# Performance work log

Hardware: AMD Instinct MI355X
Metric: run time of the kernel (lower is better)

Reference implementation:

```python
import jax, jax.numpy as jnp
import numpy as np

N_NODES = 100000
N_EDGES = 1600000
IN_FEATS = 128
OUT_FEATS = 128


def setup_inputs() -> dict:
    key = jax.random.key(0)
    ks = jax.random.split(key, 8)
    feat = jax.random.normal(ks[0], (N_NODES, IN_FEATS), dtype=jnp.float32)
    weight = jax.random.normal(ks[1], (IN_FEATS, OUT_FEATS), dtype=jnp.float32) * (1.0 / np.sqrt(IN_FEATS))
    bias = jnp.zeros((OUT_FEATS,), dtype=jnp.float32)
    s = 1.0 / np.sqrt(OUT_FEATS)
    w_ih = jax.random.uniform(ks[2], (3 * OUT_FEATS, IN_FEATS), dtype=jnp.float32, minval=-s, maxval=s)
    w_hh = jax.random.uniform(ks[3], (3 * OUT_FEATS, OUT_FEATS), dtype=jnp.float32, minval=-s, maxval=s)
    b_ih = jax.random.uniform(ks[4], (3 * OUT_FEATS,), dtype=jnp.float32, minval=-s, maxval=s)
    b_hh = jax.random.uniform(ks[5], (3 * OUT_FEATS,), dtype=jnp.float32, minval=-s, maxval=s)
    src = jax.random.randint(ks[6], (N_EDGES,), 0, N_NODES, dtype=jnp.int32)
    dst = jax.random.randint(ks[7], (N_EDGES,), 0, N_NODES, dtype=jnp.int32)
    return {"feat": feat, "weight": weight, "bias": bias,
            "w_ih": w_ih, "w_hh": w_hh, "b_ih": b_ih, "b_hh": b_hh,
            "src": src, "dst": dst}


def reference(feat, weight, bias, w_ih, w_hh, b_ih, b_hh, src, dst):
    n = feat.shape[0]
    # symmetric-ish GCN norm: in-degree^{-1/2}, clamped at 1
    deg = jax.ops.segment_sum(jnp.ones(dst.shape, feat.dtype), dst, num_segments=n)
    norm = jnp.power(jnp.clip(deg, 1.0, None), -0.5)[:, None]  # [N,1]
    featn = feat * norm
    # copy_src + sum aggregation (SpMM via gather + segment_sum), then matmul
    agg = jax.ops.segment_sum(featn[src], dst, num_segments=n)  # [N, in]
    rst = agg @ weight                                           # [N, out]
    rst = rst * norm + bias
    # GRUCell(input=featn, hidden=rst)
    gi = featn @ w_ih.T + b_ih   # [N, 3*out]
    gh = rst @ w_hh.T + b_hh     # [N, 3*out]
    i_r, i_z, i_n = jnp.split(gi, 3, axis=1)
    h_r, h_z, h_n = jnp.split(gh, 3, axis=1)
    r = jax.nn.sigmoid(i_r + h_r)
    z = jax.nn.sigmoid(i_z + h_z)
    nn_ = jnp.tanh(i_n + r * h_n)
    return (1.0 - z) * nn_ + z * rst
```

## Files before the change

kernel.cpp:

```cpp
#include <hip/hip_runtime.h>
#include <hip/hip_bf16.h>
#include <math.h>

#define N_NODES 100000
#define N_EDGES 1600000
#define F 128


#define WS_FEATN_OFF 8001536
#define WS_WTI_OFF   59201536
#define WS_WTH_OFF   59398144
#define WS_NEED_FULL (WS_WTH_OFF + 196608)

__global__ __launch_bounds__(256) void k_degree(const int* __restrict__ dst,
                                                int* __restrict__ deg) {
    int i = blockIdx.x * 256 + threadIdx.x;
    if (i < N_EDGES) atomicAdd(&deg[dst[i]], 1);
}

#define SCAN_B 512
#define SCAN_NB 196

__global__ __launch_bounds__(SCAN_B) void k_scan1(const int* __restrict__ deg,
                                                  int* __restrict__ bsum) {
    __shared__ int s[SCAN_B];
    int t = threadIdx.x;
    int i = blockIdx.x * SCAN_B + t;
    s[t] = (i < N_NODES) ? deg[i] : 0;
    __syncthreads();
    for (int o = SCAN_B / 2; o > 0; o >>= 1) {
        if (t < o) s[t] += s[t + o];
        __syncthreads();
    }
    if (t == 0) bsum[blockIdx.x] = s[0];
}

__global__ __launch_bounds__(256) void k_scan2(int* __restrict__ bsum) {
    __shared__ int s[256];
    int t = threadIdx.x;
    int v = (t < SCAN_NB) ? bsum[t] : 0;
    s[t] = v;
    __syncthreads();
    for (int o = 1; o < 256; o <<= 1) {
        int x = (t >= o) ? s[t - o] : 0;
        __syncthreads();
        s[t] += x;
        __syncthreads();
    }
    if (t < SCAN_NB) bsum[t] = (t == 0) ? 0 : s[t - 1];
}

__global__ __launch_bounds__(SCAN_B) void k_scan3(const int* __restrict__ deg,
                                                  const int* __restrict__ bsum,
                                                  int* __restrict__ offs,
                                                  float* __restrict__ norm,
                                                  int* __restrict__ cursor) {
    __shared__ int s[SCAN_B];
    int t = threadIdx.x;
    int i = blockIdx.x * SCAN_B + t;
    int v = (i < N_NODES) ? deg[i] : 0;
    s[t] = v;
    __syncthreads();
    for (int o = 1; o < SCAN_B; o <<= 1) {
        int x = (t >= o) ? s[t - o] : 0;
        __syncthreads();
        s[t] += x;
        __syncthreads();
    }
    if (i < N_NODES) {
        offs[i] = bsum[blockIdx.x] + s[t] - v;
        norm[i] = rsqrtf(fmaxf((float)v, 1.0f));
        cursor[i] = 0;
    }
    if (blockIdx.x == 0 && t == 0) offs[N_NODES] = N_EDGES;
}

__global__ __launch_bounds__(256) void k_fill(const int* __restrict__ src,
                                              const int* __restrict__ dst,
                                              const int* __restrict__ offs,
                                              int* __restrict__ cursor,
                                              int* __restrict__ ssrc) {
    int i = blockIdx.x * 256 + threadIdx.x;
    if (i < N_EDGES) {
        int d = dst[i];
        int p = atomicAdd(&cursor[d], 1);
        ssrc[offs[d] + p] = src[i];
    }
}

__global__ __launch_bounds__(256) void k_featn(const float* __restrict__ feat,
                                               const float* __restrict__ norm,
                                               float* __restrict__ featn) {
    int idx = blockIdx.x * 256 + threadIdx.x;
    int row = idx >> 5;
    float nv = norm[row];
    float4 v = ((const float4*)feat)[idx];
    v.x *= nv; v.y *= nv; v.z *= nv; v.w *= nv;
    ((float4*)featn)[idx] = v;
}

__global__ __launch_bounds__(256) void k_wt(const float* __restrict__ w_ih,
                                            const float* __restrict__ w_hh,
                                            float* __restrict__ wT_ih,
                                            float* __restrict__ wT_hh) {
    __shared__ float tile[32][33];
    int b = blockIdx.x;
    const float* w = (b < 48) ? w_ih : w_hh;
    float* wT      = (b < 48) ? wT_ih : wT_hh;
    int bb = (b < 48) ? b : b - 48;
    int rt = bb >> 2, ct = bb & 3;
    int r0 = rt * 32, c0 = ct * 32;
    int tr = threadIdx.x >> 5, tc = threadIdx.x & 31;
#pragma unroll
    for (int i = 0; i < 32; i += 8)
        tile[tr + i][tc] = w[(r0 + tr + i) * 128 + c0 + tc];
    __syncthreads();
#pragma unroll
    for (int i = 0; i < 32; i += 8)
        wT[(c0 + tr + i) * 384 + r0 + tc] = tile[tc][tr + i];
}

#define ROWS 8
template <bool PRE>
__global__ __launch_bounds__(256, 4) void k_fused(
    const float* __restrict__ fsrc, const float* __restrict__ norm,
    const int* __restrict__ offs, const int* __restrict__ ssrc,
    const float* __restrict__ W, const float* __restrict__ bias,
    const float* __restrict__ wih_, const float* __restrict__ whh_,
    const float* __restrict__ b_ih, const float* __restrict__ b_hh,
    float* __restrict__ out) {
    __shared__ float sagg[ROWS][F];
    __shared__ float sfeat[ROWS][F];
    __shared__ float srst[ROWS][F];
    __shared__ float snorm[ROWS];

    int t = threadIdx.x;
    int row0 = blockIdx.x * ROWS;

    if (t < ROWS) snorm[t] = norm[row0 + t];
    {
        int r = t >> 5, c = t & 31;
        float4 f = ((const float4*)(fsrc + (size_t)(row0 + r) * F))[c];
        if (!PRE) {
            float nv = norm[row0 + r];
            f.x *= nv; f.y *= nv; f.z *= nv; f.w *= nv;
        }
        ((float4*)&sfeat[r][0])[c] = f;
    }

    int wave = t >> 6, lane = t & 63;
    int hf = lane >> 5, sub = lane & 31;
    for (int ln = wave; ln < ROWS; ln += 4) {
        int node = row0 + ln;
        int beg = offs[node], end = offs[node + 1];
        float4 acc = make_float4(0.f, 0.f, 0.f, 0.f);
        int e = beg;
        for (; e + 7 < end; e += 8) {
            int s0 = ssrc[e + 0 + hf];
            int s1 = ssrc[e + 2 + hf];
            int s2 = ssrc[e + 4 + hf];
            int s3 = ssrc[e + 6 + hf];
            float4 v0 = *(const float4*)(fsrc + (size_t)s0 * F + sub * 4);
            float4 v1 = *(const float4*)(fsrc + (size_t)s1 * F + sub * 4);
            float4 v2 = *(const float4*)(fsrc + (size_t)s2 * F + sub * 4);
            float4 v3 = *(const float4*)(fsrc + (size_t)s3 * F + sub * 4);
            if (PRE) {
                acc.x += (v0.x + v1.x) + (v2.x + v3.x);
                acc.y += (v0.y + v1.y) + (v2.y + v3.y);
                acc.z += (v0.z + v1.z) + (v2.z + v3.z);
                acc.w += (v0.w + v1.w) + (v2.w + v3.w);
            } else {
                float n0 = norm[s0], n1 = norm[s1], n2 = norm[s2], n3 = norm[s3];
                acc.x = fmaf(v0.x, n0, acc.x); acc.y = fmaf(v0.y, n0, acc.y);
                acc.z = fmaf(v0.z, n0, acc.z); acc.w = fmaf(v0.w, n0, acc.w);
                acc.x = fmaf(v1.x, n1, acc.x); acc.y = fmaf(v1.y, n1, acc.y);
                acc.z = fmaf(v1.z, n1, acc.z); acc.w = fmaf(v1.w, n1, acc.w);
                acc.x = fmaf(v2.x, n2, acc.x); acc.y = fmaf(v2.y, n2, acc.y);
                acc.z = fmaf(v2.z, n2, acc.z); acc.w = fmaf(v2.w, n2, acc.w);
                acc.x = fmaf(v3.x, n3, acc.x); acc.y = fmaf(v3.y, n3, acc.y);
                acc.z = fmaf(v3.z, n3, acc.z); acc.w = fmaf(v3.w, n3, acc.w);
            }
        }
        for (; e < end; e += 2) {
            int edge = e + hf;
            if (edge < end) {
                int s0 = ssrc[edge];
                float4 v0 = *(const float4*)(fsrc + (size_t)s0 * F + sub * 4);
                float n0 = PRE ? 1.0f : norm[s0];
                acc.x = fmaf(v0.x, n0, acc.x); acc.y = fmaf(v0.y, n0, acc.y);
                acc.z = fmaf(v0.z, n0, acc.z); acc.w = fmaf(v0.w, n0, acc.w);
            }
        }
        acc.x += __shfl_xor(acc.x, 32, 64);
        acc.y += __shfl_xor(acc.y, 32, 64);
        acc.z += __shfl_xor(acc.z, 32, 64);
        acc.w += __shfl_xor(acc.w, 32, 64);
        if (hf == 0) *(float4*)&sagg[ln][sub * 4] = acc;
    }
    __syncthreads();

    int j = t & 127;
    int rg = (t >> 7) * 4;
    {
        float acc[4] = {0, 0, 0, 0};
        for (int k = 0; k < F; k += 4) {
            float w0 = W[(k + 0) * F + j];
            float w1 = W[(k + 1) * F + j];
            float w2 = W[(k + 2) * F + j];
            float w3 = W[(k + 3) * F + j];
#pragma unroll
            for (int r = 0; r < 4; ++r) {
                float4 a = *(const float4*)&sagg[rg + r][k];
                acc[r] = fmaf(a.x, w0, acc[r]);
                acc[r] = fmaf(a.y, w1, acc[r]);
                acc[r] = fmaf(a.z, w2, acc[r]);
                acc[r] = fmaf(a.w, w3, acc[r]);
            }
        }
        float bj = bias[j];
#pragma unroll
        for (int r = 0; r < 4; ++r) {
            srst[rg + r][j] = acc[r] * snorm[rg + r] + bj;
        }
    }
    __syncthreads();

    float accr[4] = {0, 0, 0, 0};
    float accz[4] = {0, 0, 0, 0};
    float accin[4] = {0, 0, 0, 0};
    float acchn[4] = {0, 0, 0, 0};

    if (PRE) {
        for (int k = 0; k < F; k += 4) {
            float wir[4], wiz[4], win[4], whr[4], whz[4], whn[4];
#pragma unroll
            for (int kk = 0; kk < 4; ++kk) {
                const float* wik = wih_ + (size_t)(k + kk) * 384 + j;
                const float* whk = whh_ + (size_t)(k + kk) * 384 + j;
                wir[kk] = wik[0]; wiz[kk] = wik[128]; win[kk] = wik[256];
                whr[kk] = whk[0]; whz[kk] = whk[128]; whn[kk] = whk[256];
            }
#pragma unroll
            for (int r = 0; r < 4; ++r) {
                float4 a = *(const float4*)&sfeat[rg + r][k];
                float4 h = *(const float4*)&srst[rg + r][k];
                accr[r] = fmaf(a.x, wir[0], accr[r]); accr[r] = fmaf(h.x, whr[0], accr[r]);
                accr[r] = fmaf(a.y, wir[1], accr[r]); accr[r] = fmaf(h.y, whr[1], accr[r]);
                accr[r] = fmaf(a.z, wir[2], accr[r]); accr[r] = fmaf(h.z, whr[2], accr[r]);
                accr[r] = fmaf(a.w, wir[3], accr[r]); accr[r] = fmaf(h.w, whr[3], accr[r]);
                accz[r] = fmaf(a.x, wiz[0], accz[r]); accz[r] = fmaf(h.x, whz[0], accz[r]);
                accz[r] = fmaf(a.y, wiz[1], accz[r]); accz[r] = fmaf(h.y, whz[1], accz[r]);
                accz[r] = fmaf(a.z, wiz[2], accz[r]); accz[r] = fmaf(h.z, whz[2], accz[r]);
                accz[r] = fmaf(a.w, wiz[3], accz[r]); accz[r] = fmaf(h.w, whz[3], accz[r]);
                accin[r] = fmaf(a.x, win[0], accin[r]); accin[r] = fmaf(a.y, win[1], accin[r]);
                accin[r] = fmaf(a.z, win[2], accin[r]); accin[r] = fmaf(a.w, win[3], accin[r]);
                acchn[r] = fmaf(h.x, whn[0], acchn[r]); acchn[r] = fmaf(h.y, whn[1], acchn[r]);
                acchn[r] = fmaf(h.z, whn[2], acchn[r]); acchn[r] = fmaf(h.w, whn[3], acchn[r]);
            }
        }
    } else {
        const float* wirp = wih_ + (size_t)(j + 0) * F;
        const float* wizp = wih_ + (size_t)(j + 128) * F;
        const float* winp = wih_ + (size_t)(j + 256) * F;
        const float* whrp = whh_ + (size_t)(j + 0) * F;
        const float* whzp = whh_ + (size_t)(j + 128) * F;
        const float* whnp = whh_ + (size_t)(j + 256) * F;
        for (int k = 0; k < F; k += 4) {
            float4 bir = *(const float4*)(wirp + k);
            float4 biz = *(const float4*)(wizp + k);
            float4 bin = *(const float4*)(winp + k);
            float4 bhr = *(const float4*)(whrp + k);
            float4 bhz = *(const float4*)(whzp + k);
            float4 bhn = *(const float4*)(whnp + k);
#pragma unroll
            for (int r = 0; r < 4; ++r) {
                float4 a = *(const float4*)&sfeat[rg + r][k];
                float4 h = *(const float4*)&srst[rg + r][k];
                accr[r] = fmaf(a.x, bir.x, accr[r]); accr[r] = fmaf(h.x, bhr.x, accr[r]);
                accr[r] = fmaf(a.y, bir.y, accr[r]); accr[r] = fmaf(h.y, bhr.y, accr[r]);
                accr[r] = fmaf(a.z, bir.z, accr[r]); accr[r] = fmaf(h.z, bhr.z, accr[r]);
                accr[r] = fmaf(a.w, bir.w, accr[r]); accr[r] = fmaf(h.w, bhr.w, accr[r]);
                accz[r] = fmaf(a.x, biz.x, accz[r]); accz[r] = fmaf(h.x, bhz.x, accz[r]);
                accz[r] = fmaf(a.y, biz.y, accz[r]); accz[r] = fmaf(h.y, bhz.y, accz[r]);
                accz[r] = fmaf(a.z, biz.z, accz[r]); accz[r] = fmaf(h.z, bhz.z, accz[r]);
                accz[r] = fmaf(a.w, biz.w, accz[r]); accz[r] = fmaf(h.w, bhz.w, accz[r]);
                accin[r] = fmaf(a.x, bin.x, accin[r]); accin[r] = fmaf(a.y, bin.y, accin[r]);
                accin[r] = fmaf(a.z, bin.z, accin[r]); accin[r] = fmaf(a.w, bin.w, accin[r]);
                acchn[r] = fmaf(h.x, bhn.x, acchn[r]); acchn[r] = fmaf(h.y, bhn.y, acchn[r]);
                acchn[r] = fmaf(h.z, bhn.z, acchn[r]); acchn[r] = fmaf(h.w, bhn.w, acchn[r]);
            }
        }
    }

    float Brz = b_ih[j] + b_hh[j];
    float Bzz = b_ih[j + 128] + b_hh[j + 128];
    float Bin = b_ih[j + 256], Bhn = b_hh[j + 256];
#pragma unroll
    for (int r = 0; r < 4; ++r) {
        int row = row0 + rg + r;
        float rr = 1.0f / (1.0f + __expf(-(accr[r] + Brz)));
        float zz = 1.0f / (1.0f + __expf(-(accz[r] + Bzz)));
        float nn = tanhf(accin[r] + Bin + rr * (acchn[r] + Bhn));
        float rstv = srst[rg + r][j];
        out[(size_t)row * F + j] = (1.0f - zz) * nn + zz * rstv;
    }
}

extern "C" void kernel_launch(void* const* d_in, const int* in_sizes, int n_in,
                              void* d_out, int out_size, void* d_ws, size_t ws_size,
                              hipStream_t stream) {
    const float* feat   = (const float*)d_in[0];
    const float* weight = (const float*)d_in[1];
    const float* bias   = (const float*)d_in[2];
    const float* w_ih   = (const float*)d_in[3];
    const float* w_hh   = (const float*)d_in[4];
    const float* b_ih   = (const float*)d_in[5];
    const float* b_hh   = (const float*)d_in[6];
    const int*   src    = (const int*)d_in[7];
    const int*   dst    = (const int*)d_in[8];
    float* out = (float*)d_out;

    char* ws = (char*)d_ws;
    int*   deg    = (int*)(ws + 0);
    float* norm   = (float*)(ws + 400000);
    int*   offs   = (int*)(ws + 800000);
    int*   cursor = (int*)(ws + 1200016);
    int*   ssrc   = (int*)(ws + 1600016);
    int*   bsum   = (int*)(ws + 8000016);
    float* featn  = (float*)(ws + WS_FEATN_OFF);
    float* wT_ih  = (float*)(ws + WS_WTI_OFF);
    float* wT_hh  = (float*)(ws + WS_WTH_OFF);

    hipMemsetAsync(deg, 0, N_NODES * sizeof(int), stream);

    k_degree<<<(N_EDGES + 255) / 256, 256, 0, stream>>>(dst, deg);
    k_scan1<<<SCAN_NB, SCAN_B, 0, stream>>>(deg, bsum);
    k_scan2<<<1, 256, 0, stream>>>(bsum);
    k_scan3<<<SCAN_NB, SCAN_B, 0, stream>>>(deg, bsum, offs, norm, cursor);
    k_fill<<<(N_EDGES + 255) / 256, 256, 0, stream>>>(src, dst, offs, cursor, ssrc);

    if (ws_size >= WS_NEED_FULL) {
        k_wt<<<96, 256, 0, stream>>>(w_ih, w_hh, wT_ih, wT_hh);
        k_featn<<<(N_NODES * F / 4) / 256, 256, 0, stream>>>(feat, norm, featn);
        k_fused<true><<<N_NODES / ROWS, 256, 0, stream>>>(featn, norm, offs, ssrc,
                                                          weight, bias, wT_ih, wT_hh,
                                                          b_ih, b_hh, out);
    } else {
        k_fused<false><<<N_NODES / ROWS, 256, 0, stream>>>(feat, norm, offs, ssrc,
                                                           weight, bias, w_ih, w_hh,
                                                           b_ih, b_hh, out);
    }
}
```

Measured before the change: 830.6 us.

## Pack GRU weights into interleaved float4/float2 layout and double rows per block

```diff
diff --git a/kernel.cpp b/kernel.cpp
--- a/kernel.cpp
+++ b/kernel.cpp
@@ -8,9 +8,9 @@
 
 
 #define WS_FEATN_OFF 8001536
-#define WS_WTI_OFF   59201536
-#define WS_WTH_OFF   59398144
-#define WS_NEED_FULL (WS_WTH_OFF + 196608)
+#define WS_WPA_OFF   59201536
+#define WS_WPB_OFF   59463680
+#define WS_NEED_FULL (WS_WPB_OFF + 131072)
 
 __global__ __launch_bounds__(256) void k_degree(const int* __restrict__ dst,
                                                 int* __restrict__ deg) {
@@ -99,33 +99,31 @@
     ((float4*)featn)[idx] = v;
 }
 
-__global__ __launch_bounds__(256) void k_wt(const float* __restrict__ w_ih,
-                                            const float* __restrict__ w_hh,
-                                            float* __restrict__ wT_ih,
-                                            float* __restrict__ wT_hh) {
-    __shared__ float tile[32][33];
-    int b = blockIdx.x;
-    const float* w = (b < 48) ? w_ih : w_hh;
-    float* wT      = (b < 48) ? wT_ih : wT_hh;
-    int bb = (b < 48) ? b : b - 48;
-    int rt = bb >> 2, ct = bb & 3;
-    int r0 = rt * 32, c0 = ct * 32;
-    int tr = threadIdx.x >> 5, tc = threadIdx.x & 31;
-#pragma unroll
-    for (int i = 0; i < 32; i += 8)
-        tile[tr + i][tc] = w[(r0 + tr + i) * 128 + c0 + tc];
-    __syncthreads();
-#pragma unroll
-    for (int i = 0; i < 32; i += 8)
-        wT[(c0 + tr + i) * 384 + r0 + tc] = tile[tc][tr + i];
-}
-
-#define ROWS 8
+__global__ __launch_bounds__(256) void k_pack(const float* __restrict__ w_ih,
+                                              const float* __restrict__ w_hh,
+                                              float4* __restrict__ wPa,
+                                              float2* __restrict__ wPb) {
+    int idx = blockIdx.x * 256 + threadIdx.x;
+    int k = idx >> 7, j = idx & 127;
+    float4 a;
+    a.x = w_ih[j * 128 + k];
+    a.y = w_ih[(j + 128) * 128 + k];
+    a.z = w_ih[(j + 256) * 128 + k];
+    a.w = w_hh[j * 128 + k];
+    float2 b;
+    b.x = w_hh[(j + 128) * 128 + k];
+    b.y = w_hh[(j + 256) * 128 + k];
+    wPa[idx] = a;
+    wPb[idx] = b;
+}
+
+#define ROWS 16
 template <bool PRE>
-__global__ __launch_bounds__(256, 4) void k_fused(
+__global__ __launch_bounds__(512, 4) void k_fused(
     const float* __restrict__ fsrc, const float* __restrict__ norm,
     const int* __restrict__ offs, const int* __restrict__ ssrc,
     const float* __restrict__ W, const float* __restrict__ bias,
+    const float4* __restrict__ wPa_, const float2* __restrict__ wPb_,
     const float* __restrict__ wih_, const float* __restrict__ whh_,
     const float* __restrict__ b_ih, const float* __restrict__ b_hh,
     float* __restrict__ out) {
@@ -150,7 +148,7 @@
 
     int wave = t >> 6, lane = t & 63;
     int hf = lane >> 5, sub = lane & 31;
-    for (int ln = wave; ln < ROWS; ln += 4) {
+    for (int ln = wave; ln < ROWS; ln += 8) {
         int node = row0 + ln;
         int beg = offs[node], end = offs[node + 1];
         float4 acc = make_float4(0.f, 0.f, 0.f, 0.f);
@@ -231,31 +229,33 @@
     float acchn[4] = {0, 0, 0, 0};
 
     if (PRE) {
+        const float4* pa = wPa_ + j;
+        const float2* pb = wPb_ + j;
         for (int k = 0; k < F; k += 4) {
-            float wir[4], wiz[4], win[4], whr[4], whz[4], whn[4];
-#pragma unroll
-            for (int kk = 0; kk < 4; ++kk) {
-                const float* wik = wih_ + (size_t)(k + kk) * 384 + j;
-                const float* whk = whh_ + (size_t)(k + kk) * 384 + j;
-                wir[kk] = wik[0]; wiz[kk] = wik[128]; win[kk] = wik[256];
-                whr[kk] = whk[0]; whz[kk] = whk[128]; whn[kk] = whk[256];
-            }
+            float4 A0 = pa[(k + 0) * 128];
+            float4 A1 = pa[(k + 1) * 128];
+            float4 A2 = pa[(k + 2) * 128];
+            float4 A3 = pa[(k + 3) * 128];
+            float2 B0 = pb[(k + 0) * 128];
+            float2 B1 = pb[(k + 1) * 128];
+            float2 B2 = pb[(k + 2) * 128];
+            float2 B3 = pb[(k + 3) * 128];
 #pragma unroll
             for (int r = 0; r < 4; ++r) {
                 float4 a = *(const float4*)&sfeat[rg + r][k];
                 float4 h = *(const float4*)&srst[rg + r][k];
-                accr[r] = fmaf(a.x, wir[0], accr[r]); accr[r] = fmaf(h.x, whr[0], accr[r]);
-                accr[r] = fmaf(a.y, wir[1], accr[r]); accr[r] = fmaf(h.y, whr[1], accr[r]);
-                accr[r] = fmaf(a.z, wir[2], accr[r]); accr[r] = fmaf(h.z, whr[2], accr[r]);
-                accr[r] = fmaf(a.w, wir[3], accr[r]); accr[r] = fmaf(h.w, whr[3], accr[r]);
-                accz[r] = fmaf(a.x, wiz[0], accz[r]); accz[r] = fmaf(h.x, whz[0], accz[r]);
-                accz[r] = fmaf(a.y, wiz[1], accz[r]); accz[r] = fmaf(h.y, whz[1], accz[r]);
-                accz[r] = fmaf(a.z, wiz[2], accz[r]); accz[r] = fmaf(h.z, whz[2], accz[r]);
-                accz[r] = fmaf(a.w, wiz[3], accz[r]); accz[r] = fmaf(h.w, whz[3], accz[r]);
-                accin[r] = fmaf(a.x, win[0], accin[r]); accin[r] = fmaf(a.y, win[1], accin[r]);
-                accin[r] = fmaf(a.z, win[2], accin[r]); accin[r] = fmaf(a.w, win[3], accin[r]);
-                acchn[r] = fmaf(h.x, whn[0], acchn[r]); acchn[r] = fmaf(h.y, whn[1], acchn[r]);
-                acchn[r] = fmaf(h.z, whn[2], acchn[r]); acchn[r] = fmaf(h.w, whn[3], acchn[r]);
+                accr[r] = fmaf(a.x, A0.x, accr[r]); accr[r] = fmaf(h.x, A0.w, accr[r]);
+                accr[r] = fmaf(a.y, A1.x, accr[r]); accr[r] = fmaf(h.y, A1.w, accr[r]);
+                accr[r] = fmaf(a.z, A2.x, accr[r]); accr[r] = fmaf(h.z, A2.w, accr[r]);
+                accr[r] = fmaf(a.w, A3.x, accr[r]); accr[r] = fmaf(h.w, A3.w, accr[r]);
+                accz[r] = fmaf(a.x, A0.y, accz[r]); accz[r] = fmaf(h.x, B0.x, accz[r]);
+                accz[r] = fmaf(a.y, A1.y, accz[r]); accz[r] = fmaf(h.y, B1.x, accz[r]);
+                accz[r] = fmaf(a.z, A2.y, accz[r]); accz[r] = fmaf(h.z, B2.x, accz[r]);
+                accz[r] = fmaf(a.w, A3.y, accz[r]); accz[r] = fmaf(h.w, B3.x, accz[r]);
+                accin[r] = fmaf(a.x, A0.z, accin[r]); accin[r] = fmaf(a.y, A1.z, accin[r]);
+                accin[r] = fmaf(a.z, A2.z, accin[r]); accin[r] = fmaf(a.w, A3.z, accin[r]);
+                acchn[r] = fmaf(h.x, B0.y, acchn[r]); acchn[r] = fmaf(h.y, B1.y, acchn[r]);
+                acchn[r] = fmaf(h.z, B2.y, acchn[r]); acchn[r] = fmaf(h.w, B3.y, acchn[r]);
             }
         }
     } else {
@@ -321,15 +321,15 @@
     float* out = (float*)d_out;
 
     char* ws = (char*)d_ws;
-    int*   deg    = (int*)(ws + 0);
-    float* norm   = (float*)(ws + 400000);
-    int*   offs   = (int*)(ws + 800000);
-    int*   cursor = (int*)(ws + 1200016);
-    int*   ssrc   = (int*)(ws + 1600016);
-    int*   bsum   = (int*)(ws + 8000016);
-    float* featn  = (float*)(ws + WS_FEATN_OFF);
-    float* wT_ih  = (float*)(ws + WS_WTI_OFF);
-    float* wT_hh  = (float*)(ws + WS_WTH_OFF);
+    int*    deg    = (int*)(ws + 0);
+    float*  norm   = (float*)(ws + 400000);
+    int*    offs   = (int*)(ws + 800000);
+    int*    cursor = (int*)(ws + 1200016);
+    int*    ssrc   = (int*)(ws + 1600016);
+    int*    bsum   = (int*)(ws + 8000016);
+    float*  featn  = (float*)(ws + WS_FEATN_OFF);
+    float4* wPa    = (float4*)(ws + WS_WPA_OFF);
+    float2* wPb    = (float2*)(ws + WS_WPB_OFF);
 
     hipMemsetAsync(deg, 0, N_NODES * sizeof(int), stream);
 
@@ -340,14 +340,16 @@
     k_fill<<<(N_EDGES + 255) / 256, 256, 0, stream>>>(src, dst, offs, cursor, ssrc);
 
     if (ws_size >= WS_NEED_FULL) {
-        k_wt<<<96, 256, 0, stream>>>(w_ih, w_hh, wT_ih, wT_hh);
+        k_pack<<<64, 256, 0, stream>>>(w_ih, w_hh, wPa, wPb);
         k_featn<<<(N_NODES * F / 4) / 256, 256, 0, stream>>>(feat, norm, featn);
-        k_fused<true><<<N_NODES / ROWS, 256, 0, stream>>>(featn, norm, offs, ssrc,
-                                                          weight, bias, wT_ih, wT_hh,
+        k_fused<true><<<N_NODES / ROWS, 512, 0, stream>>>(featn, norm, offs, ssrc,
+                                                          weight, bias, wPa, wPb,
+                                                          nullptr, nullptr,
                                                           b_ih, b_hh, out);
     } else {
-        k_fused<false><<<N_NODES / ROWS, 256, 0, stream>>>(feat, norm, offs, ssrc,
-                                                           weight, bias, w_ih, w_hh,
+        k_fused<false><<<N_NODES / ROWS, 512, 0, stream>>>(feat, norm, offs, ssrc,
+                                                           weight, bias, nullptr, nullptr,
+                                                           w_ih, w_hh,
                                                            b_ih, b_hh, out);
     }
 }
```

Result: no change. 823.1 us (-0.9%).

## Use split-bf16 MFMA for GCN and GRU matmuls with 32-row tiles

Applied to the files above, without the earlier changes.

```diff
diff --git a/kernel.cpp b/kernel.cpp
--- a/kernel.cpp
+++ b/kernel.cpp
@@ -8,9 +8,32 @@
 
 
 #define WS_FEATN_OFF 8001536
-#define WS_WTI_OFF   59201536
-#define WS_WTH_OFF   59398144
-#define WS_NEED_FULL (WS_WTH_OFF + 196608)
+#define WS_WIHH 1200016
+#define WS_WIHL 1298320
+#define WS_WTH  59201536
+#define WS_WTL  59234304
+#define WS_WHHH 59267072
+#define WS_WHHL 59365376
+
+using s8v = __attribute__((ext_vector_type(8))) short;
+using f4v = __attribute__((ext_vector_type(4))) float;
+
+__device__ __forceinline__ void bsplit(float x, unsigned short& h, unsigned short& l) {
+    unsigned bx = __float_as_uint(x);
+    unsigned rh = bx + 0x7FFFu + ((bx >> 16) & 1u);
+    h = (unsigned short)(rh >> 16);
+    float fh = __uint_as_float(((unsigned)h) << 16);
+    float lo = x - fh;
+    unsigned bl = __float_as_uint(lo);
+    unsigned rl = bl + 0x7FFFu + ((bl >> 16) & 1u);
+    l = (unsigned short)(rl >> 16);
+}
+
+__device__ __forceinline__ unsigned long long pack4(unsigned short a, unsigned short b,
+                                                    unsigned short c, unsigned short d) {
+    return (unsigned long long)a | ((unsigned long long)b << 16) |
+           ((unsigned long long)c << 32) | ((unsigned long long)d << 48);
+}
 
 __global__ __launch_bounds__(256) void k_degree(const int* __restrict__ dst,
                                                 int* __restrict__ deg) {
@@ -99,58 +122,68 @@
     ((float4*)featn)[idx] = v;
 }
 
-__global__ __launch_bounds__(256) void k_wt(const float* __restrict__ w_ih,
-                                            const float* __restrict__ w_hh,
-                                            float* __restrict__ wT_ih,
-                                            float* __restrict__ wT_hh) {
-    __shared__ float tile[32][33];
-    int b = blockIdx.x;
-    const float* w = (b < 48) ? w_ih : w_hh;
-    float* wT      = (b < 48) ? wT_ih : wT_hh;
-    int bb = (b < 48) ? b : b - 48;
-    int rt = bb >> 2, ct = bb & 3;
-    int r0 = rt * 32, c0 = ct * 32;
-    int tr = threadIdx.x >> 5, tc = threadIdx.x & 31;
-#pragma unroll
-    for (int i = 0; i < 32; i += 8)
-        tile[tr + i][tc] = w[(r0 + tr + i) * 128 + c0 + tc];
-    __syncthreads();
-#pragma unroll
-    for (int i = 0; i < 32; i += 8)
-        wT[(c0 + tr + i) * 384 + r0 + tc] = tile[tc][tr + i];
-}
-
-#define ROWS 8
-template <bool PRE>
-__global__ __launch_bounds__(256, 4) void k_fused(
-    const float* __restrict__ fsrc, const float* __restrict__ norm,
+__global__ __launch_bounds__(256) void k_packw(const float* __restrict__ weight,
+                                               const float* __restrict__ w_ih,
+                                               const float* __restrict__ w_hh,
+                                               unsigned short* __restrict__ WtH,
+                                               unsigned short* __restrict__ WtL,
+                                               unsigned short* __restrict__ wihH,
+                                               unsigned short* __restrict__ wihL,
+                                               unsigned short* __restrict__ whhH,
+                                               unsigned short* __restrict__ whhL) {
+    int idx = blockIdx.x * 256 + threadIdx.x;
+    unsigned short h, l;
+    if (idx < 16384) {
+        int n = idx >> 7, k = idx & 127;
+        bsplit(weight[k * 128 + n], h, l);
+        WtH[idx] = h; WtL[idx] = l;
+    } else if (idx < 65536) {
+        int i2 = idx - 16384;
+        bsplit(w_ih[i2], h, l);
+        wihH[i2] = h; wihL[i2] = l;
+    } else {
+        int i2 = idx - 65536;
+        bsplit(w_hh[i2], h, l);
+        whhH[i2] = h; whhL[i2] = l;
+    }
+}
+
+#define ROWS 32
+__global__ __launch_bounds__(512, 2) void k_fused(
+    const float* __restrict__ featn, const float* __restrict__ norm,
     const int* __restrict__ offs, const int* __restrict__ ssrc,
-    const float* __restrict__ W, const float* __restrict__ bias,
-    const float* __restrict__ wih_, const float* __restrict__ whh_,
-    const float* __restrict__ b_ih, const float* __restrict__ b_hh,
-    float* __restrict__ out) {
-    __shared__ float sagg[ROWS][F];
-    __shared__ float sfeat[ROWS][F];
-    __shared__ float srst[ROWS][F];
+    const unsigned short* __restrict__ WtH, const unsigned short* __restrict__ WtL,
+    const unsigned short* __restrict__ wihH, const unsigned short* __restrict__ wihL,
+    const unsigned short* __restrict__ whhH, const unsigned short* __restrict__ whhL,
+    const float* __restrict__ bias, const float* __restrict__ b_ih,
+    const float* __restrict__ b_hh, float* __restrict__ out) {
+    __shared__ __align__(16) unsigned short sfH[4096], sfL[4096];
+    __shared__ __align__(16) unsigned short sgH[4096], sgL[4096];
+    __shared__ __align__(16) unsigned short srH[4096], srL[4096];
     __shared__ float snorm[ROWS];
 
     int t = threadIdx.x;
+    int l = t & 63, w = t >> 6, g = l >> 4;
     int row0 = blockIdx.x * ROWS;
 
     if (t < ROWS) snorm[t] = norm[row0 + t];
-    {
-        int r = t >> 5, c = t & 31;
-        float4 f = ((const float4*)(fsrc + (size_t)(row0 + r) * F))[c];
-        if (!PRE) {
-            float nv = norm[row0 + r];
-            f.x *= nv; f.y *= nv; f.z *= nv; f.w *= nv;
-        }
-        ((float4*)&sfeat[r][0])[c] = f;
-    }
-
-    int wave = t >> 6, lane = t & 63;
-    int hf = lane >> 5, sub = lane & 31;
-    for (int ln = wave; ln < ROWS; ln += 4) {
+
+#pragma unroll
+    for (int u = 0; u < 2; ++u) {
+        int idx = u * 512 + t;
+        int r = idx >> 5, c = idx & 31;
+        float4 f = ((const float4*)(featn + (size_t)(row0 + r) * F))[c];
+        int k0 = c * 4;
+        int pos = (r >> 4) * 2048 + (k0 >> 3) * 128 + (r & 15) * 8 + (k0 & 7);
+        unsigned short h0, l0, h1, l1, h2, l2, h3, l3;
+        bsplit(f.x, h0, l0); bsplit(f.y, h1, l1);
+        bsplit(f.z, h2, l2); bsplit(f.w, h3, l3);
+        *(unsigned long long*)(&sfH[pos]) = pack4(h0, h1, h2, h3);
+        *(unsigned long long*)(&sfL[pos]) = pack4(l0, l1, l2, l3);
+    }
+
+    int hf = l >> 5, sub = l & 31;
+    for (int ln = w; ln < ROWS; ln += 8) {
         int node = row0 + ln;
         int beg = offs[node], end = offs[node + 1];
         float4 acc = make_float4(0.f, 0.f, 0.f, 0.f);
@@ -160,149 +193,125 @@
             int s1 = ssrc[e + 2 + hf];
             int s2 = ssrc[e + 4 + hf];
             int s3 = ssrc[e + 6 + hf];
-            float4 v0 = *(const float4*)(fsrc + (size_t)s0 * F + sub * 4);
-            float4 v1 = *(const float4*)(fsrc + (size_t)s1 * F + sub * 4);
-            float4 v2 = *(const float4*)(fsrc + (size_t)s2 * F + sub * 4);
-            float4 v3 = *(const float4*)(fsrc + (size_t)s3 * F + sub * 4);
-            if (PRE) {
-                acc.x += (v0.x + v1.x) + (v2.x + v3.x);
-                acc.y += (v0.y + v1.y) + (v2.y + v3.y);
-                acc.z += (v0.z + v1.z) + (v2.z + v3.z);
-                acc.w += (v0.w + v1.w) + (v2.w + v3.w);
-            } else {
-                float n0 = norm[s0], n1 = norm[s1], n2 = norm[s2], n3 = norm[s3];
-                acc.x = fmaf(v0.x, n0, acc.x); acc.y = fmaf(v0.y, n0, acc.y);
-                acc.z = fmaf(v0.z, n0, acc.z); acc.w = fmaf(v0.w, n0, acc.w);
-                acc.x = fmaf(v1.x, n1, acc.x); acc.y = fmaf(v1.y, n1, acc.y);
-                acc.z = fmaf(v1.z, n1, acc.z); acc.w = fmaf(v1.w, n1, acc.w);
-                acc.x = fmaf(v2.x, n2, acc.x); acc.y = fmaf(v2.y, n2, acc.y);
-                acc.z = fmaf(v2.z, n2, acc.z); acc.w = fmaf(v2.w, n2, acc.w);
-                acc.x = fmaf(v3.x, n3, acc.x); acc.y = fmaf(v3.y, n3, acc.y);
-                acc.z = fmaf(v3.z, n3, acc.z); acc.w = fmaf(v3.w, n3, acc.w);
-            }
+            float4 v0 = *(const float4*)(featn + (size_t)s0 * F + sub * 4);
+            float4 v1 = *(const float4*)(featn + (size_t)s1 * F + sub * 4);
+            float4 v2 = *(const float4*)(featn + (size_t)s2 * F + sub * 4);
+            float4 v3 = *(const float4*)(featn + (size_t)s3 * F + sub * 4);
+            acc.x += (v0.x + v1.x) + (v2.x + v3.x);
+            acc.y += (v0.y + v1.y) + (v2.y + v3.y);
+            acc.z += (v0.z + v1.z) + (v2.z + v3.z);
+            acc.w += (v0.w + v1.w) + (v2.w + v3.w);
         }
         for (; e < end; e += 2) {
             int edge = e + hf;
             if (edge < end) {
                 int s0 = ssrc[edge];
-                float4 v0 = *(const float4*)(fsrc + (size_t)s0 * F + sub * 4);
-                float n0 = PRE ? 1.0f : norm[s0];
-                acc.x = fmaf(v0.x, n0, acc.x); acc.y = fmaf(v0.y, n0, acc.y);
-                acc.z = fmaf(v0.z, n0, acc.z); acc.w = fmaf(v0.w, n0, acc.w);
+                float4 v0 = *(const float4*)(featn + (size_t)s0 * F + sub * 4);
+                acc.x += v0.x; acc.y += v0.y; acc.z += v0.z; acc.w += v0.w;
             }
         }
         acc.x += __shfl_xor(acc.x, 32, 64);
         acc.y += __shfl_xor(acc.y, 32, 64);
         acc.z += __shfl_xor(acc.z, 32, 64);
         acc.w += __shfl_xor(acc.w, 32, 64);
-        if (hf == 0) *(float4*)&sagg[ln][sub * 4] = acc;
-    }
-    __syncthreads();
-
-    int j = t & 127;
-    int rg = (t >> 7) * 4;
-    {
-        float acc[4] = {0, 0, 0, 0};
-        for (int k = 0; k < F; k += 4) {
-            float w0 = W[(k + 0) * F + j];
-            float w1 = W[(k + 1) * F + j];
-            float w2 = W[(k + 2) * F + j];
-            float w3 = W[(k + 3) * F + j];
-#pragma unroll
-            for (int r = 0; r < 4; ++r) {
-                float4 a = *(const float4*)&sagg[rg + r][k];
-                acc[r] = fmaf(a.x, w0, acc[r]);
-                acc[r] = fmaf(a.y, w1, acc[r]);
-                acc[r] = fmaf(a.z, w2, acc[r]);
-                acc[r] = fmaf(a.w, w3, acc[r]);
-            }
-        }
-        float bj = bias[j];
-#pragma unroll
-        for (int r = 0; r < 4; ++r) {
-            srst[rg + r][j] = acc[r] * snorm[rg + r] + bj;
-        }
-    }
-    __syncthreads();
-
-    float accr[4] = {0, 0, 0, 0};
-    float accz[4] = {0, 0, 0, 0};
-    float accin[4] = {0, 0, 0, 0};
-    float acchn[4] = {0, 0, 0, 0};
-
-    if (PRE) {
-        for (int k = 0; k < F; k += 4) {
-            float wir[4], wiz[4], win[4], whr[4], whz[4], whn[4];
-#pragma unroll
-            for (int kk = 0; kk < 4; ++kk) {
-                const float* wik = wih_ + (size_t)(k + kk) * 384 + j;
-                const float* whk = whh_ + (size_t)(k + kk) * 384 + j;
-                wir[kk] = wik[0]; wiz[kk] = wik[128]; win[kk] = wik[256];
-                whr[kk] = whk[0]; whz[kk] = whk[128]; whn[kk] = whk[256];
-            }
-#pragma unroll
-            for (int r = 0; r < 4; ++r) {
-                float4 a = *(const float4*)&sfeat[rg + r][k];
-                float4 h = *(const float4*)&srst[rg + r][k];
-                accr[r] = fmaf(a.x, wir[0], accr[r]); accr[r] = fmaf(h.x, whr[0], accr[r]);
-                accr[r] = fmaf(a.y, wir[1], accr[r]); accr[r] = fmaf(h.y, whr[1], accr[r]);
-                accr[r] = fmaf(a.z, wir[2], accr[r]); accr[r] = fmaf(h.z, whr[2], accr[r]);
-                accr[r] = fmaf(a.w, wir[3], accr[r]); accr[r] = fmaf(h.w, whr[3], accr[r]);
-                accz[r] = fmaf(a.x, wiz[0], accz[r]); accz[r] = fmaf(h.x, whz[0], accz[r]);
-                accz[r] = fmaf(a.y, wiz[1], accz[r]); accz[r] = fmaf(h.y, whz[1], accz[r]);
-                accz[r] = fmaf(a.z, wiz[2], accz[r]); accz[r] = fmaf(h.z, whz[2], accz[r]);
-                accz[r] = fmaf(a.w, wiz[3], accz[r]); accz[r] = fmaf(h.w, whz[3], accz[r]);
-                accin[r] = fmaf(a.x, win[0], accin[r]); accin[r] = fmaf(a.y, win[1], accin[r]);
-                accin[r] = fmaf(a.z, win[2], accin[r]); accin[r] = fmaf(a.w, win[3], accin[r]);
-                acchn[r] = fmaf(h.x, whn[0], acchn[r]); acchn[r] = fmaf(h.y, whn[1], acchn[r]);
-                acchn[r] = fmaf(h.z, whn[2], acchn[r]); acchn[r] = fmaf(h.w, whn[3], acchn[r]);
-            }
-        }
-    } else {
-        const float* wirp = wih_ + (size_t)(j + 0) * F;
-        const float* wizp = wih_ + (size_t)(j + 128) * F;
-        const float* winp = wih_ + (size_t)(j + 256) * F;
-        const float* whrp = whh_ + (size_t)(j + 0) * F;
-        const float* whzp = whh_ + (size_t)(j + 128) * F;
-        const float* whnp = whh_ + (size_t)(j + 256) * F;
-        for (int k = 0; k < F; k += 4) {
-            float4 bir = *(const float4*)(wirp + k);
-            float4 biz = *(const float4*)(wizp + k);
-            float4 bin = *(const float4*)(winp + k);
-            float4 bhr = *(const float4*)(whrp + k);
-            float4 bhz = *(const float4*)(whzp + k);
-            float4 bhn = *(const float4*)(whnp + k);
-#pragma unroll
-            for (int r = 0; r < 4; ++r) {
-                float4 a = *(const float4*)&sfeat[rg + r][k];
-                float4 h = *(const float4*)&srst[rg + r][k];
-                accr[r] = fmaf(a.x, bir.x, accr[r]); accr[r] = fmaf(h.x, bhr.x, accr[r]);
-                accr[r] = fmaf(a.y, bir.y, accr[r]); accr[r] = fmaf(h.y, bhr.y, accr[r]);
-                accr[r] = fmaf(a.z, bir.z, accr[r]); accr[r] = fmaf(h.z, bhr.z, accr[r]);
-                accr[r] = fmaf(a.w, bir.w, accr[r]); accr[r] = fmaf(h.w, bhr.w, accr[r]);
-                accz[r] = fmaf(a.x, biz.x, accz[r]); accz[r] = fmaf(h.x, bhz.x, accz[r]);
-                accz[r] = fmaf(a.y, biz.y, accz[r]); accz[r] = fmaf(h.y, bhz.y, accz[r]);
-                accz[r] = fmaf(a.z, biz.z, accz[r]); accz[r] = fmaf(h.z, bhz.z, accz[r]);
-                accz[r] = fmaf(a.w, biz.w, accz[r]); accz[r] = fmaf(h.w, bhz.w, accz[r]);
-                accin[r] = fmaf(a.x, bin.x, accin[r]); accin[r] = fmaf(a.y, bin.y, accin[r]);
-                accin[r] = fmaf(a.z, bin.z, accin[r]); accin[r] = fmaf(a.w, bin.w, accin[r]);
-                acchn[r] = fmaf(h.x, bhn.x, acchn[r]); acchn[r] = fmaf(h.y, bhn.y, acchn[r]);
-                acchn[r] = fmaf(h.z, bhn.z, acchn[r]); acchn[r] = fmaf(h.w, bhn.w, acchn[r]);
-            }
-        }
-    }
-
-    float Brz = b_ih[j] + b_hh[j];
-    float Bzz = b_ih[j + 128] + b_hh[j + 128];
-    float Bin = b_ih[j + 256], Bhn = b_hh[j + 256];
-#pragma unroll
-    for (int r = 0; r < 4; ++r) {
-        int row = row0 + rg + r;
-        float rr = 1.0f / (1.0f + __expf(-(accr[r] + Brz)));
-        float zz = 1.0f / (1.0f + __expf(-(accz[r] + Bzz)));
-        float nn = tanhf(accin[r] + Bin + rr * (acchn[r] + Bhn));
-        float rstv = srst[rg + r][j];
-        out[(size_t)row * F + j] = (1.0f - zz) * nn + zz * rstv;
+        if (hf == 0) {
+            int k0 = sub * 4;
+            int pos = (ln >> 4) * 2048 + (k0 >> 3) * 128 + (ln & 15) * 8 + (k0 & 7);
+            unsigned short h0, l0, h1, l1, h2, l2, h3, l3;
+            bsplit(acc.x, h0, l0); bsplit(acc.y, h1, l1);
+            bsplit(acc.z, h2, l2); bsplit(acc.w, h3, l3);
+            *(unsigned long long*)(&sgH[pos]) = pack4(h0, h1, h2, h3);
+            *(unsigned long long*)(&sgL[pos]) = pack4(l0, l1, l2, l3);
+        }
+    }
+    __syncthreads();
+
+    int col = w * 16 + (l & 15);
+    f4v cB0 = {0.f, 0.f, 0.f, 0.f}, cB1 = {0.f, 0.f, 0.f, 0.f};
+#pragma unroll
+    for (int pass = 0; pass < 3; ++pass) {
+        const unsigned short* As = (pass < 2) ? sgH : sgL;
+        const unsigned short* Bs = (pass == 1) ? WtL : WtH;
+#pragma unroll
+        for (int s = 0; s < 4; ++s) {
+            s8v b = *(const s8v*)(Bs + (size_t)col * 128 + 32 * s + 8 * g);
+            s8v a0 = *(const s8v*)(As + s * 512 + l * 8);
+            s8v a1 = *(const s8v*)(As + 2048 + s * 512 + l * 8);
+            cB0 = __builtin_amdgcn_mfma_f32_16x16x32_bf16(a0, b, cB0, 0, 0, 0);
+            cB1 = __builtin_amdgcn_mfma_f32_16x16x32_bf16(a1, b, cB1, 0, 0, 0);
+        }
+    }
+    float bcol = bias[col];
+    float rv0[4], rv1[4];
+#pragma unroll
+    for (int q = 0; q < 4; ++q) {
+        int ri = g * 4 + q;
+        float v0 = cB0[q] * snorm[ri] + bcol;
+        float v1 = cB1[q] * snorm[16 + ri] + bcol;
+        rv0[q] = v0; rv1[q] = v1;
+        unsigned short hh, ll;
+        int posb = (col >> 3) * 128 + ri * 8 + (col & 7);
+        bsplit(v0, hh, ll); srH[posb] = hh; srL[posb] = ll;
+        bsplit(v1, hh, ll); srH[2048 + posb] = hh; srL[2048 + posb] = ll;
+    }
+    __syncthreads();
+
+    f4v ar0 = {0.f,0.f,0.f,0.f}, ar1 = {0.f,0.f,0.f,0.f};
+    f4v az0 = {0.f,0.f,0.f,0.f}, az1 = {0.f,0.f,0.f,0.f};
+    f4v an0 = {0.f,0.f,0.f,0.f}, an1 = {0.f,0.f,0.f,0.f};
+    f4v ah0 = {0.f,0.f,0.f,0.f}, ah1 = {0.f,0.f,0.f,0.f};
+#pragma unroll
+    for (int pass = 0; pass < 3; ++pass) {
+        const unsigned short* AF = (pass < 2) ? sfH : sfL;
+        const unsigned short* AR = (pass < 2) ? srH : srL;
+        const unsigned short* WI = (pass == 1) ? wihL : wihH;
+        const unsigned short* WH = (pass == 1) ? whhL : whhH;
+#pragma unroll
+        for (int s = 0; s < 4; ++s) {
+            int koff = 32 * s + 8 * g;
+            s8v bir = *(const s8v*)(WI + (size_t)col * 128 + koff);
+            s8v biz = *(const s8v*)(WI + (size_t)(col + 128) * 128 + koff);
+            s8v bin = *(const s8v*)(WI + (size_t)(col + 256) * 128 + koff);
+            s8v bhr = *(const s8v*)(WH + (size_t)col * 128 + koff);
+            s8v bhz = *(const s8v*)(WH + (size_t)(col + 128) * 128 + koff);
+            s8v bhn = *(const s8v*)(WH + (size_t)(col + 256) * 128 + koff);
+            s8v f0 = *(const s8v*)(AF + s * 512 + l * 8);
+            s8v f1 = *(const s8v*)(AF + 2048 + s * 512 + l * 8);
+            s8v r0 = *(const s8v*)(AR + s * 512 + l * 8);
+            s8v r1 = *(const s8v*)(AR + 2048 + s * 512 + l * 8);
+            ar0 = __builtin_amdgcn_mfma_f32_16x16x32_bf16(f0, bir, ar0, 0, 0, 0);
+            ar0 = __builtin_amdgcn_mfma_f32_16x16x32_bf16(r0, bhr, ar0, 0, 0, 0);
+            ar1 = __builtin_amdgcn_mfma_f32_16x16x32_bf16(f1, bir, ar1, 0, 0, 0);
+            ar1 = __builtin_amdgcn_mfma_f32_16x16x32_bf16(r1, bhr, ar1, 0, 0, 0);
+            az0 = __builtin_amdgcn_mfma_f32_16x16x32_bf16(f0, biz, az0, 0, 0, 0);
+            az0 = __builtin_amdgcn_mfma_f32_16x16x32_bf16(r0, bhz, az0, 0, 0, 0);
+            az1 = __builtin_amdgcn_mfma_f32_16x16x32_bf16(f1, biz, az1, 0, 0, 0);
+            az1 = __builtin_amdgcn_mfma_f32_16x16x32_bf16(r1, bhz, az1, 0, 0, 0);
+            an0 = __builtin_amdgcn_mfma_f32_16x16x32_bf16(f0, bin, an0, 0, 0, 0);
+            an1 = __builtin_amdgcn_mfma_f32_16x16x32_bf16(f1, bin, an1, 0, 0, 0);
+            ah0 = __builtin_amdgcn_mfma_f32_16x16x32_bf16(r0, bhn, ah0, 0, 0, 0);
+            ah1 = __builtin_amdgcn_mfma_f32_16x16x32_bf16(r1, bhn, ah1, 0, 0, 0);
+        }
+    }
+
+    float Bir = b_ih[col], Bhr = b_hh[col];
+    float Biz = b_ih[col + 128], Bhz = b_hh[col + 128];
+    float Bin = b_ih[col + 256], Bhn = b_hh[col + 256];
+#pragma unroll
+    for (int q = 0; q < 4; ++q) {
+        int ri = g * 4 + q;
+        {
+            float rr = 1.0f / (1.0f + __expf(-(ar0[q] + Bir + Bhr)));
+            float zz = 1.0f / (1.0f + __expf(-(az0[q] + Biz + Bhz)));
+            float nn = tanhf(an0[q] + Bin + rr * (ah0[q] + Bhn));
+            out[(size_t)(row0 + ri) * F + col] = (1.0f - zz) * nn + zz * rv0[q];
+        }
+        {
+            float rr = 1.0f / (1.0f + __expf(-(ar1[q] + Bir + Bhr)));
+            float zz = 1.0f / (1.0f + __expf(-(az1[q] + Biz + Bhz)));
+            float nn = tanhf(an1[q] + Bin + rr * (ah1[q] + Bhn));
+            out[(size_t)(row0 + 16 + ri) * F + col] = (1.0f - zz) * nn + zz * rv1[q];
+        }
     }
 }
 
@@ -328,8 +337,12 @@
     int*   ssrc   = (int*)(ws + 1600016);
     int*   bsum   = (int*)(ws + 8000016);
     float* featn  = (float*)(ws + WS_FEATN_OFF);
-    float* wT_ih  = (float*)(ws + WS_WTI_OFF);
-    float* wT_hh  = (float*)(ws + WS_WTH_OFF);
+    unsigned short* wihH = (unsigned short*)(ws + WS_WIHH);
+    unsigned short* wihL = (unsigned short*)(ws + WS_WIHL);
+    unsigned short* WtH  = (unsigned short*)(ws + WS_WTH);
+    unsigned short* WtL  = (unsigned short*)(ws + WS_WTL);
+    unsigned short* whhH = (unsigned short*)(ws + WS_WHHH);
+    unsigned short* whhL = (unsigned short*)(ws + WS_WHHL);
 
     hipMemsetAsync(deg, 0, N_NODES * sizeof(int), stream);
 
@@ -338,16 +351,9 @@
     k_scan2<<<1, 256, 0, stream>>>(bsum);
     k_scan3<<<SCAN_NB, SCAN_B, 0, stream>>>(deg, bsum, offs, norm, cursor);
     k_fill<<<(N_EDGES + 255) / 256, 256, 0, stream>>>(src, dst, offs, cursor, ssrc);
-
-    if (ws_size >= WS_NEED_FULL) {
-        k_wt<<<96, 256, 0, stream>>>(w_ih, w_hh, wT_ih, wT_hh);
-        k_featn<<<(N_NODES * F / 4) / 256, 256, 0, stream>>>(feat, norm, featn);
-        k_fused<true><<<N_NODES / ROWS, 256, 0, stream>>>(featn, norm, offs, ssrc,
-                                                          weight, bias, wT_ih, wT_hh,
-                                                          b_ih, b_hh, out);
-    } else {
-        k_fused<false><<<N_NODES / ROWS, 256, 0, stream>>>(feat, norm, offs, ssrc,
-                                                           weight, bias, w_ih, w_hh,
-                                                           b_ih, b_hh, out);
-    }
-}
+    k_packw<<<448, 256, 0, stream>>>(weight, w_ih, w_hh, WtH, WtL, wihH, wihL, whhH, whhL);
+    k_featn<<<(N_NODES * F / 4) / 256, 256, 0, stream>>>(feat, norm, featn);
+    k_fused<<<N_NODES / ROWS, 512, 0, stream>>>(featn, norm, offs, ssrc,
+                                                WtH, WtL, wihH, wihL, whhH, whhL,
+                                                bias, b_ih, b_hh, out);
+}
```

After: 675.2 us. 18.7% less time.
